# Kernel optimization log

Hardware: AMD Instinct MI355X
Metric: run time of the kernel (lower is better)

The kernel has to match this reference:

```python
import jax, jax.numpy as jnp
import numpy as np

B, SIZE, OUT = 32, 2048, 2048
EPS = 1e-5

def setup_inputs() -> dict:
    key = jax.random.key(0)
    ks = jax.random.split(key, 6)
    s = SIZE ** -0.5
    return {
        "x":    jax.random.normal(ks[0], (B, SIZE), jnp.float32),
        "Wq":   jax.random.normal(ks[1], (SIZE, SIZE), jnp.float32) * s,
        "Wk":   jax.random.normal(ks[2], (SIZE, SIZE), jnp.float32) * s,
        "Wv":   jax.random.normal(ks[3], (SIZE, SIZE), jnp.float32) * s,
        "p2":   jnp.zeros((5,), jnp.float32),              # OptimActivation params (activation2)
        "Wfc2": jax.random.normal(ks[4], (OUT, SIZE), jnp.float32) * s,
        "bfc2": jnp.zeros((OUT,), jnp.float32),
        "g2":   jnp.ones((OUT,), jnp.float32),             # LayerNorm2 weight
        "b2":   jnp.zeros((OUT,), jnp.float32),            # LayerNorm2 bias
    }

def _optim_activation(x, p):
    ps = jax.nn.softmax(p)
    # swish + sine + linear branches (sigmoid/tanh branches are computed but not summed in the original)
    return jax.nn.sigmoid(x) * x * ps[0] + jnp.sin(x) * ps[1] + x * ps[2]

def _layernorm(x, g, b):
    mu = jnp.mean(x, axis=-1, keepdims=True)
    var = jnp.mean(jnp.square(x - mu), axis=-1, keepdims=True)
    return (x - mu) * jax.lax.rsqrt(var + EPS) * g + b

def reference(x, Wq, Wk, Wv, p2, Wfc2, bfc2, g2, b2):
    q = x @ Wq.T                                   # [B, S]
    k = x @ Wk.T
    v = x @ Wv.T
    bsz, s = x.shape
    att = q[:, :, None] * k[:, None, :]            # outer product  [B, S, S]
    att = jax.nn.softmax(att.reshape(bsz, s * s), axis=-1).reshape(bsz, s, s)
    valued = jnp.einsum('bij,bj->bi', att, v)      # [B, S]
    # NOTE: original's activation/fc_linear/norm result is overwritten (dead code)
    fc = _optim_activation(valued, p2)
    fc = fc @ Wfc2.T + bfc2                        # [B, OUT]
    return _layernorm(fc, g2, b2)
```

## Files before the change

### kernel.cpp

```cpp
#include <hip/hip_runtime.h>
#include <hip/hip_bf16.h>


#define S 2048
#define BATCH 32

typedef __attribute__((ext_vector_type(8))) short short8;
typedef __attribute__((ext_vector_type(4))) float f32x4;

__device__ __forceinline__ void cvt8t(const float* __restrict__ p, short8& hi, short8& lo) {
  const float4* p4 = (const float4*)p;
  float4 a = p4[0], b = p4[1];
  float v[8] = {a.x, a.y, a.z, a.w, b.x, b.y, b.z, b.w};
#pragma unroll
  for (int t = 0; t < 8; ++t) {
    union { float f; unsigned u; } x; x.f = v[t];
    hi[t] = (short)(x.u >> 16);
    union { unsigned u; float f; } h; h.u = x.u & 0xFFFF0000u;
    union { float f; unsigned u; } l; l.f = v[t] - h.f;
    lo[t] = (short)(l.u >> 16);
  }
}

__global__ __launch_bounds__(256) void k_qkv(
    const float* __restrict__ x,
    const float* __restrict__ Wq,
    const float* __restrict__ Wk,
    const float* __restrict__ Wv,
    float* __restrict__ qkvp) {
  int bid  = blockIdx.x;
  int mi   = bid >> 8;
  int kh   = (bid >> 7) & 1;
  int nblk = bid & 127;
  const float* W = (mi == 0) ? Wq : (mi == 1) ? Wk : Wv;
  float* out = qkvp + (size_t)kh * (3 * BATCH * S) + (size_t)mi * (BATCH * S);

  int tid  = threadIdx.x;
  int wave = tid >> 6;
  int lane = tid & 63;
  int lr   = lane & 15;
  int quad = lane >> 4;

  f32x4 acc0 = {0.f, 0.f, 0.f, 0.f};
  f32x4 acc1 = {0.f, 0.f, 0.f, 0.f};
  const float* wrow = W + (size_t)(nblk * 16 + lr) * S;
  const float* xr0  = x + (size_t)lr * S;
  const float* xr1  = x + (size_t)(lr + 16) * S;
  int kbase = kh * 1024 + wave * 256 + quad * 8;

#pragma unroll 2
  for (int ks = 0; ks < 8; ++ks) {
    int k0 = kbase + ks * 32;
    short8 bhi, blo, a0h, a0l, a1h, a1l;
    cvt8t(wrow + k0, bhi, blo);
    cvt8t(xr0 + k0, a0h, a0l);
    cvt8t(xr1 + k0, a1h, a1l);
    acc0 = __builtin_amdgcn_mfma_f32_16x16x32_bf16(a0h, bhi, acc0, 0, 0, 0);
    acc0 = __builtin_amdgcn_mfma_f32_16x16x32_bf16(a0l, bhi, acc0, 0, 0, 0);
    acc0 = __builtin_amdgcn_mfma_f32_16x16x32_bf16(a0h, blo, acc0, 0, 0, 0);
    acc1 = __builtin_amdgcn_mfma_f32_16x16x32_bf16(a1h, bhi, acc1, 0, 0, 0);
    acc1 = __builtin_amdgcn_mfma_f32_16x16x32_bf16(a1l, bhi, acc1, 0, 0, 0);
    acc1 = __builtin_amdgcn_mfma_f32_16x16x32_bf16(a1h, blo, acc1, 0, 0, 0);
  }

  __shared__ float red[4][64][8];
#pragma unroll
  for (int r = 0; r < 4; ++r) {
    red[wave][lane][r]     = acc0[r];
    red[wave][lane][4 + r] = acc1[r];
  }
  __syncthreads();
  if (tid < 64) {
    int lq = tid >> 4, lc = tid & 15;
    int n = nblk * 16 + lc;
#pragma unroll
    for (int r = 0; r < 8; ++r) {
      float s = red[0][tid][r] + red[1][tid][r] + red[2][tid][r] + red[3][tid][r];
      int m = (r < 4) ? (lq * 4 + r) : (16 + lq * 4 + (r - 4));
      out[m * S + n] = s;
    }
  }
}

__global__ __launch_bounds__(256) void k_attn(
    const float* __restrict__ qkvp, float* __restrict__ Tout, float* __restrict__ Spart) {
  int b    = blockIdx.x >> 5;
  int iblk = blockIdx.x & 31;
  const float* qA = qkvp + (size_t)b * S;
  const float* kA = qA + BATCH * S;
  const float* vA = qA + 2 * BATCH * S;
  const float* qB = qA + 3 * BATCH * S;
  const float* kB = kA + 3 * BATCH * S;
  const float* vB = vA + 3 * BATCH * S;

  __shared__ __align__(16) float2 kv[S];
  __shared__ float qsh[64];
  __shared__ float redmx[4][4];
  __shared__ float redST[256][2];
  __shared__ float Msh;

  int tid = threadIdx.x;
  float qmx = -1e30f, qmn = 1e30f, kmx = -1e30f, kmn = 1e30f;
  for (int idx = tid; idx < S; idx += 256) {
    float kk = kA[idx] + kB[idx];
    float vv = vA[idx] + vB[idx];
    float qq = qA[idx] + qB[idx];
    kv[idx] = make_float2(kk, vv);
    if ((idx >> 6) == iblk) qsh[idx & 63] = qq;
    qmx = fmaxf(qmx, qq); qmn = fminf(qmn, qq);
    kmx = fmaxf(kmx, kk); kmn = fminf(kmn, kk);
  }
  for (int off = 32; off; off >>= 1) {
    qmx = fmaxf(qmx, __shfl_xor(qmx, off));
    qmn = fminf(qmn, __shfl_xor(qmn, off));
    kmx = fmaxf(kmx, __shfl_xor(kmx, off));
    kmn = fminf(kmn, __shfl_xor(kmn, off));
  }
  int wave = tid >> 6, lane = tid & 63;
  if (lane == 0) {
    redmx[wave][0] = qmx; redmx[wave][1] = qmn;
    redmx[wave][2] = kmx; redmx[wave][3] = kmn;
  }
  __syncthreads();
  if (tid == 0) {
    float a = redmx[0][0], bn = redmx[0][1], c = redmx[0][2], d = redmx[0][3];
    for (int w = 1; w < 4; ++w) {
      a = fmaxf(a, redmx[w][0]); bn = fminf(bn, redmx[w][1]);
      c = fmaxf(c, redmx[w][2]); d = fminf(d, redmx[w][3]);
    }
    Msh = fmaxf(fmaxf(a * c, a * d), fmaxf(bn * c, bn * d));
  }
  __syncthreads();
  float M = Msh;

  const float LOG2E = 1.4426950408889634f;
  float aa = qsh[lane] * LOG2E;
  float cc = -M * LOG2E;
  float S0 = 0.f, S1 = 0.f, T0 = 0.f, T1 = 0.f;
  int j0 = wave * 512;
#pragma unroll 4
  for (int j = j0; j < j0 + 512; j += 4) {
    float4 p0 = *(const float4*)&kv[j];
    float4 p1 = *(const float4*)&kv[j + 2];
    float e0 = __builtin_amdgcn_exp2f(fmaf(aa, p0.x, cc));
    float e1 = __builtin_amdgcn_exp2f(fmaf(aa, p0.z, cc));
    float e2 = __builtin_amdgcn_exp2f(fmaf(aa, p1.x, cc));
    float e3 = __builtin_amdgcn_exp2f(fmaf(aa, p1.z, cc));
    S0 += e0 + e1;
    S1 += e2 + e3;
    T0 = fmaf(e0, p0.y, fmaf(e1, p0.w, T0));
    T1 = fmaf(e2, p1.y, fmaf(e3, p1.w, T1));
  }
  redST[tid][0] = S0 + S1;
  redST[tid][1] = T0 + T1;
  __syncthreads();
  if (tid < 64) {
    float Sf = redST[tid][0] + redST[tid + 64][0] + redST[tid + 128][0] + redST[tid + 192][0];
    float Tf = redST[tid][1] + redST[tid + 64][1] + redST[tid + 128][1] + redST[tid + 192][1];
    Tout[b * S + iblk * 64 + tid] = Tf;
    for (int off = 32; off; off >>= 1) Sf += __shfl_xor(Sf, off);
    if (tid == 0) Spart[b * 32 + iblk] = Sf;
  }
}

__global__ __launch_bounds__(256) void k_act(
    const float* __restrict__ Tin, const float* __restrict__ Spart,
    const float* __restrict__ p2, float* __restrict__ fc) {
  int tid = threadIdx.x;
  int gid = blockIdx.x * 256 + tid;
  int b = gid >> 11;
  __shared__ float Zsh;
  if (tid < 64) {
    float zv = (tid < 32) ? Spart[b * 32 + tid] : 0.f;
    for (int off = 32; off; off >>= 1) zv += __shfl_xor(zv, off);
    if (tid == 0) Zsh = zv;
  }
  __syncthreads();
  float Z = Zsh;

  const float LOG2E = 1.4426950408889634f;
  float p[5];
  float mx = -1e30f;
#pragma unroll
  for (int t = 0; t < 5; ++t) { p[t] = p2[t]; mx = fmaxf(mx, p[t]); }
  float se = 0.f;
#pragma unroll
  for (int t = 0; t < 5; ++t) { p[t] = __builtin_amdgcn_exp2f((p[t] - mx) * LOG2E); se += p[t]; }
  float inv = 1.f / se;
  float val = Tin[gid] / Z;
  float sig = __builtin_amdgcn_rcpf(1.f + __builtin_amdgcn_exp2f(-val * LOG2E));
  float sn  = __builtin_amdgcn_sinf(val * 0.15915494309189535f);
  fc[gid] = sig * val * (p[0] * inv) + sn * (p[1] * inv) + val * (p[2] * inv);
}

__global__ __launch_bounds__(512) void k_fc(
    const float* __restrict__ fc,
    const float* __restrict__ W,
    float* __restrict__ yp) {
  int bid  = blockIdx.x;
  int kh   = bid >> 7;
  int nblk = bid & 127;
  int tid  = threadIdx.x;
  int wave = tid >> 6;
  int lane = tid & 63;
  int lr   = lane & 15;
  int quad = lane >> 4;

  f32x4 acc0 = {0.f, 0.f, 0.f, 0.f};
  f32x4 acc1 = {0.f, 0.f, 0.f, 0.f};
  const float* wrow = W + (size_t)(nblk * 16 + lr) * S;
  const float* xr0  = fc + (size_t)lr * S;
  const float* xr1  = fc + (size_t)(lr + 16) * S;
  int kbase = kh * 1024 + wave * 128 + quad * 8;

#pragma unroll
  for (int ks = 0; ks < 4; ++ks) {
    int k0 = kbase + ks * 32;
    short8 bhi, blo, a0h, a0l, a1h, a1l;
    cvt8t(wrow + k0, bhi, blo);
    cvt8t(xr0 + k0, a0h, a0l);
    cvt8t(xr1 + k0, a1h, a1l);
    acc0 = __builtin_amdgcn_mfma_f32_16x16x32_bf16(a0h, bhi, acc0, 0, 0, 0);
    acc0 = __builtin_amdgcn_mfma_f32_16x16x32_bf16(a0l, bhi, acc0, 0, 0, 0);
    acc0 = __builtin_amdgcn_mfma_f32_16x16x32_bf16(a0h, blo, acc0, 0, 0, 0);
    acc1 = __builtin_amdgcn_mfma_f32_16x16x32_bf16(a1h, bhi, acc1, 0, 0, 0);
    acc1 = __builtin_amdgcn_mfma_f32_16x16x32_bf16(a1l, bhi, acc1, 0, 0, 0);
    acc1 = __builtin_amdgcn_mfma_f32_16x16x32_bf16(a1h, blo, acc1, 0, 0, 0);
  }

  __shared__ float red[8][64][8];
#pragma unroll
  for (int r = 0; r < 4; ++r) {
    red[wave][lane][r]     = acc0[r];
    red[wave][lane][4 + r] = acc1[r];
  }
  __syncthreads();
  if (tid < 64) {
    int lq = tid >> 4, lc = tid & 15;
    int n = nblk * 16 + lc;
#pragma unroll
    for (int r = 0; r < 8; ++r) {
      float s = 0.f;
#pragma unroll
      for (int w = 0; w < 8; ++w) s += red[w][tid][r];
      int m = (r < 4) ? (lq * 4 + r) : (16 + lq * 4 + (r - 4));
      yp[(size_t)kh * BATCH * S + m * S + n] = s;
    }
  }
}

__global__ __launch_bounds__(256) void k_ln(
    const float* __restrict__ yp, const float* __restrict__ bias,
    const float* __restrict__ g, const float* __restrict__ bb,
    float* __restrict__ out) {
  int b = blockIdx.x;
  const float* r0 = yp + (size_t)b * S;
  const float* r1 = r0 + BATCH * S;
  float t8[8];
  float s = 0.f, s2 = 0.f;
#pragma unroll
  for (int it = 0; it < 8; ++it) {
    int i = threadIdx.x + it * 256;
    float t = r0[i] + r1[i] + bias[i];
    t8[it] = t;
    s += t; s2 += t * t;
  }
  for (int off = 32; off; off >>= 1) {
    s  += __shfl_xor(s, off);
    s2 += __shfl_xor(s2, off);
  }
  __shared__ float rs[4], rs2[4];
  __shared__ float mu_s, r_s;
  int wave = threadIdx.x >> 6, lane = threadIdx.x & 63;
  if (lane == 0) { rs[wave] = s; rs2[wave] = s2; }
  __syncthreads();
  if (threadIdx.x == 0) {
    float S1 = rs[0] + rs[1] + rs[2] + rs[3];
    float S2 = rs2[0] + rs2[1] + rs2[2] + rs2[3];
    float mu = S1 / (float)S;
    float var = S2 / (float)S - mu * mu;
    mu_s = mu;
    r_s = rsqrtf(var + 1e-5f);
  }
  __syncthreads();
  float mu = mu_s, r = r_s;
#pragma unroll
  for (int it = 0; it < 8; ++it) {
    int i = threadIdx.x + it * 256;
    out[b * S + i] = (t8[it] - mu) * r * g[i] + bb[i];
  }
}

extern "C" void kernel_launch(void* const* d_in, const int* in_sizes, int n_in,
                              void* d_out, int out_size, void* d_ws, size_t ws_size,
                              hipStream_t stream) {
  (void)in_sizes; (void)n_in; (void)out_size; (void)ws_size;
  const float* x    = (const float*)d_in[0];
  const float* Wq   = (const float*)d_in[1];
  const float* Wk   = (const float*)d_in[2];
  const float* Wv   = (const float*)d_in[3];
  const float* p2   = (const float*)d_in[4];
  const float* Wfc2 = (const float*)d_in[5];
  const float* bfc2 = (const float*)d_in[6];
  const float* g2   = (const float*)d_in[7];
  const float* b2   = (const float*)d_in[8];
  float* out = (float*)d_out;

  float* qkvp  = (float*)d_ws;
  float* T     = qkvp + 2 * 3 * BATCH * S;
  float* Spart = T + BATCH * S;
  float* fc    = Spart + BATCH * 32;
  float* yp    = fc + BATCH * S;

  k_qkv<<<768, 256, 0, stream>>>(x, Wq, Wk, Wv, qkvp);
  k_attn<<<1024, 256, 0, stream>>>(qkvp, T, Spart);
  k_act<<<256, 256, 0, stream>>>(T, Spart, p2, fc);
  k_fc<<<256, 512, 0, stream>>>(fc, Wfc2, yp);
  k_ln<<<32, 256, 0, stream>>>(yp, bfc2, g2, b2, out);
}
```

Before: 152.7 us.

## Process two queries per lane with packed FMA in attention; split FC K four ways

The attention kernel now uses 512-thread blocks that each cover 128 query rows. Each lane handles two queries, so every K/V pair loaded from LDS is reused twice, and the q*k+c and e*v updates use packed two-wide FMA. This halves the number of blocks that redundantly reload and reduce the full K/V vectors. The FC GEMM moves from a two-way to a four-way K split with 256-thread blocks, doubling the block count, and layernorm sums four partial outputs instead of two.

```diff
diff --git a/kernel.cpp b/kernel.cpp
--- a/kernel.cpp
+++ b/kernel.cpp
@@ -7,6 +7,17 @@
 
 typedef __attribute__((ext_vector_type(8))) short short8;
 typedef __attribute__((ext_vector_type(4))) float f32x4;
+typedef __attribute__((ext_vector_type(2))) float f32x2;
+
+#if __has_builtin(__builtin_elementwise_fma)
+__device__ __forceinline__ f32x2 pkfma(f32x2 a, f32x2 b, f32x2 c) {
+  return __builtin_elementwise_fma(a, b, c);
+}
+#else
+__device__ __forceinline__ f32x2 pkfma(f32x2 a, f32x2 b, f32x2 c) {
+  f32x2 r; r.x = fmaf(a.x, b.x, c.x); r.y = fmaf(a.y, b.y, c.y); return r;
+}
+#endif
 
 __device__ __forceinline__ void cvt8t(const float* __restrict__ p, short8& hi, short8& lo) {
   const float4* p4 = (const float4*)p;
@@ -82,10 +93,10 @@
   }
 }
 
-__global__ __launch_bounds__(256) void k_attn(
+__global__ __launch_bounds__(512) void k_attn(
     const float* __restrict__ qkvp, float* __restrict__ Tout, float* __restrict__ Spart) {
-  int b    = blockIdx.x >> 5;
-  int iblk = blockIdx.x & 31;
+  int b    = blockIdx.x >> 4;
+  int iblk = blockIdx.x & 15;
   const float* qA = qkvp + (size_t)b * S;
   const float* kA = qA + BATCH * S;
   const float* vA = qA + 2 * BATCH * S;
@@ -94,19 +105,20 @@
   const float* vB = vA + 3 * BATCH * S;
 
   __shared__ __align__(16) float2 kv[S];
-  __shared__ float qsh[64];
-  __shared__ float redmx[4][4];
-  __shared__ float redST[256][2];
+  __shared__ float qsh[128];
+  __shared__ float redmx[8][4];
+  __shared__ f32x2 redT[512];
+  __shared__ float redS[512];
   __shared__ float Msh;
 
   int tid = threadIdx.x;
   float qmx = -1e30f, qmn = 1e30f, kmx = -1e30f, kmn = 1e30f;
-  for (int idx = tid; idx < S; idx += 256) {
+  for (int idx = tid; idx < S; idx += 512) {
     float kk = kA[idx] + kB[idx];
     float vv = vA[idx] + vB[idx];
     float qq = qA[idx] + qB[idx];
     kv[idx] = make_float2(kk, vv);
-    if ((idx >> 6) == iblk) qsh[idx & 63] = qq;
+    if ((idx >> 7) == iblk) qsh[idx & 127] = qq;
     qmx = fmaxf(qmx, qq); qmn = fminf(qmn, qq);
     kmx = fmaxf(kmx, kk); kmn = fminf(kmn, kk);
   }
@@ -124,7 +136,7 @@
   __syncthreads();
   if (tid == 0) {
     float a = redmx[0][0], bn = redmx[0][1], c = redmx[0][2], d = redmx[0][3];
-    for (int w = 1; w < 4; ++w) {
+    for (int w = 1; w < 8; ++w) {
       a = fmaxf(a, redmx[w][0]); bn = fminf(bn, redmx[w][1]);
       c = fmaxf(c, redmx[w][2]); d = fminf(d, redmx[w][3]);
     }
@@ -134,32 +146,45 @@
   float M = Msh;
 
   const float LOG2E = 1.4426950408889634f;
-  float aa = qsh[lane] * LOG2E;
-  float cc = -M * LOG2E;
-  float S0 = 0.f, S1 = 0.f, T0 = 0.f, T1 = 0.f;
-  int j0 = wave * 512;
+  f32x2 aa = {qsh[lane] * LOG2E, qsh[lane + 64] * LOG2E};
+  float ccs = -M * LOG2E;
+  f32x2 cc = {ccs, ccs};
+  f32x2 Sp = {0.f, 0.f}, Sq = {0.f, 0.f};
+  f32x2 Tp = {0.f, 0.f}, Tq = {0.f, 0.f};
+  int j0 = wave * 256;
 #pragma unroll 4
-  for (int j = j0; j < j0 + 512; j += 4) {
-    float4 p0 = *(const float4*)&kv[j];
-    float4 p1 = *(const float4*)&kv[j + 2];
-    float e0 = __builtin_amdgcn_exp2f(fmaf(aa, p0.x, cc));
-    float e1 = __builtin_amdgcn_exp2f(fmaf(aa, p0.z, cc));
-    float e2 = __builtin_amdgcn_exp2f(fmaf(aa, p1.x, cc));
-    float e3 = __builtin_amdgcn_exp2f(fmaf(aa, p1.z, cc));
-    S0 += e0 + e1;
-    S1 += e2 + e3;
-    T0 = fmaf(e0, p0.y, fmaf(e1, p0.w, T0));
-    T1 = fmaf(e2, p1.y, fmaf(e3, p1.w, T1));
-  }
-  redST[tid][0] = S0 + S1;
-  redST[tid][1] = T0 + T1;
-  __syncthreads();
+  for (int j = j0; j < j0 + 256; j += 2) {
+    float4 p = *(const float4*)&kv[j];
+    f32x2 kk0 = {p.x, p.x}, vv0 = {p.y, p.y};
+    f32x2 kk1 = {p.z, p.z}, vv1 = {p.w, p.w};
+    f32x2 a0 = pkfma(aa, kk0, cc);
+    f32x2 a1 = pkfma(aa, kk1, cc);
+    f32x2 e0 = {__builtin_amdgcn_exp2f(a0.x), __builtin_amdgcn_exp2f(a0.y)};
+    f32x2 e1 = {__builtin_amdgcn_exp2f(a1.x), __builtin_amdgcn_exp2f(a1.y)};
+    Sp += e0;
+    Sq += e1;
+    Tp = pkfma(e0, vv0, Tp);
+    Tq = pkfma(e1, vv1, Tq);
+  }
+  redT[tid] = Tp + Tq;
+  redS[tid] = Sp.x + Sp.y + Sq.x + Sq.y;
+  __syncthreads();
+  if (tid < 128) {
+    int l = tid & 63, hi = tid >> 6;
+    float Tf = 0.f;
+#pragma unroll
+    for (int w = 0; w < 8; ++w) {
+      f32x2 t = redT[w * 64 + l];
+      Tf += hi ? t.y : t.x;
+    }
+    Tout[b * S + iblk * 128 + tid] = Tf;
+  }
   if (tid < 64) {
-    float Sf = redST[tid][0] + redST[tid + 64][0] + redST[tid + 128][0] + redST[tid + 192][0];
-    float Tf = redST[tid][1] + redST[tid + 64][1] + redST[tid + 128][1] + redST[tid + 192][1];
-    Tout[b * S + iblk * 64 + tid] = Tf;
+    float Sf = 0.f;
+#pragma unroll
+    for (int w = 0; w < 8; ++w) Sf += redS[w * 64 + tid];
     for (int off = 32; off; off >>= 1) Sf += __shfl_xor(Sf, off);
-    if (tid == 0) Spart[b * 32 + iblk] = Sf;
+    if (tid == 0) Spart[b * 16 + iblk] = Sf;
   }
 }
 
@@ -171,7 +196,7 @@
   int b = gid >> 11;
   __shared__ float Zsh;
   if (tid < 64) {
-    float zv = (tid < 32) ? Spart[b * 32 + tid] : 0.f;
+    float zv = (tid < 16) ? Spart[b * 16 + tid] : 0.f;
     for (int off = 32; off; off >>= 1) zv += __shfl_xor(zv, off);
     if (tid == 0) Zsh = zv;
   }
@@ -193,12 +218,12 @@
   fc[gid] = sig * val * (p[0] * inv) + sn * (p[1] * inv) + val * (p[2] * inv);
 }
 
-__global__ __launch_bounds__(512) void k_fc(
+__global__ __launch_bounds__(256) void k_fc(
     const float* __restrict__ fc,
     const float* __restrict__ W,
     float* __restrict__ yp) {
   int bid  = blockIdx.x;
-  int kh   = bid >> 7;
+  int kq   = bid >> 7;
   int nblk = bid & 127;
   int tid  = threadIdx.x;
   int wave = tid >> 6;
@@ -211,7 +236,7 @@
   const float* wrow = W + (size_t)(nblk * 16 + lr) * S;
   const float* xr0  = fc + (size_t)lr * S;
   const float* xr1  = fc + (size_t)(lr + 16) * S;
-  int kbase = kh * 1024 + wave * 128 + quad * 8;
+  int kbase = kq * 512 + wave * 128 + quad * 8;
 
 #pragma unroll
   for (int ks = 0; ks < 4; ++ks) {
@@ -228,7 +253,7 @@
     acc1 = __builtin_amdgcn_mfma_f32_16x16x32_bf16(a1h, blo, acc1, 0, 0, 0);
   }
 
-  __shared__ float red[8][64][8];
+  __shared__ float red[4][64][8];
 #pragma unroll
   for (int r = 0; r < 4; ++r) {
     red[wave][lane][r]     = acc0[r];
@@ -240,11 +265,9 @@
     int n = nblk * 16 + lc;
 #pragma unroll
     for (int r = 0; r < 8; ++r) {
-      float s = 0.f;
-#pragma unroll
-      for (int w = 0; w < 8; ++w) s += red[w][tid][r];
+      float s = red[0][tid][r] + red[1][tid][r] + red[2][tid][r] + red[3][tid][r];
       int m = (r < 4) ? (lq * 4 + r) : (16 + lq * 4 + (r - 4));
-      yp[(size_t)kh * BATCH * S + m * S + n] = s;
+      yp[(size_t)kq * BATCH * S + m * S + n] = s;
     }
   }
 }
@@ -256,12 +279,14 @@
   int b = blockIdx.x;
   const float* r0 = yp + (size_t)b * S;
   const float* r1 = r0 + BATCH * S;
+  const float* r2 = r1 + BATCH * S;
+  const float* r3 = r2 + BATCH * S;
   float t8[8];
   float s = 0.f, s2 = 0.f;
 #pragma unroll
   for (int it = 0; it < 8; ++it) {
     int i = threadIdx.x + it * 256;
-    float t = r0[i] + r1[i] + bias[i];
+    float t = (r0[i] + r1[i]) + (r2[i] + r3[i]) + bias[i];
     t8[it] = t;
     s += t; s2 += t * t;
   }
@@ -309,12 +334,12 @@
   float* qkvp  = (float*)d_ws;
   float* T     = qkvp + 2 * 3 * BATCH * S;
   float* Spart = T + BATCH * S;
-  float* fc    = Spart + BATCH * 32;
+  float* fc    = Spart + BATCH * 16;
   float* yp    = fc + BATCH * S;
 
   k_qkv<<<768, 256, 0, stream>>>(x, Wq, Wk, Wv, qkvp);
-  k_attn<<<1024, 256, 0, stream>>>(qkvp, T, Spart);
+  k_attn<<<512, 512, 0, stream>>>(qkvp, T, Spart);
   k_act<<<256, 256, 0, stream>>>(T, Spart, p2, fc);
-  k_fc<<<256, 512, 0, stream>>>(fc, Wfc2, yp);
+  k_fc<<<512, 256, 0, stream>>>(fc, Wfc2, yp);
   k_ln<<<32, 256, 0, stream>>>(yp, bfc2, g2, b2, out);
 }
```

Measured after the change: 150.7 us. About the same (-1.3%).
